# Kernel tuning notes

Measured on AMD Instinct MI355X. Metric: run time of the kernel, lower is better.

Reference implementation:

```python
import jax, jax.numpy as jnp
import numpy as np
from jax import lax

B, S, H = 2, 512, 2048          # batch, seq, hidden_size
I = 768                          # moe_intermediate_size
E = 64                           # num_experts
K = 8                            # num_experts_per_tok (top_k)


def setup_inputs() -> dict:
    key = jax.random.key(0)
    k1, k2, k3, k4 = jax.random.split(key, 4)
    hidden_states = jax.random.normal(k1, (B, S, H), jnp.float32)
    gate_weight = jax.random.normal(k2, (E, H), jnp.float32) * 0.02
    gate_up_weights = jax.random.normal(k3, (E, H, 2 * I), jnp.float32) * 0.02
    down_weights = jax.random.normal(k4, (E, I, H), jnp.float32) * 0.02
    return {
        "hidden_states": hidden_states,
        "gate_weight": gate_weight,
        "gate_up_weights": gate_up_weights,
        "down_weights": down_weights,
    }


def reference(hidden_states, gate_weight, gate_up_weights, down_weights):
    orig_shape = hidden_states.shape
    x = hidden_states.reshape(-1, H)          # [T, H]
    T = x.shape[0]

    # Router: softmax in fp32, top-k, renormalize (norm_topk_prob=True)
    logits = x @ gate_weight.T                # [T, E]
    probs = jax.nn.softmax(logits.astype(jnp.float32), axis=-1)
    routing_weights, selected_experts = lax.top_k(probs, K)   # [T, K]
    wsum = routing_weights.sum(axis=-1, keepdims=True)
    wsum = jnp.where(wsum == 0, 1.0, wsum)
    routing_weights = (routing_weights / wsum).astype(x.dtype)

    # Dense combine matrix [T, E]: zero weight for unselected experts.
    combine = jnp.zeros((T, E), x.dtype).at[
        jnp.arange(T)[:, None], selected_experts
    ].add(routing_weights)

    # Scan over experts; each step is one batched GEMM over all tokens,
    # masked/weighted by the combine weights (same math as per-token loop).
    def body(acc, ws):
        wgu, wd, we = ws                      # [H,2I], [I,H], [T]
        gu = x @ wgu                          # [T, 2I]
        gate, up = jnp.split(gu, 2, axis=-1)  # [T, I] each
        act = jax.nn.silu(gate) * up          # SwiGLU
        out = act @ wd                        # [T, H]
        return acc + we[:, None] * out, None

    init = jnp.zeros_like(x)
    final, _ = lax.scan(body, init, (gate_up_weights, down_weights, combine.T))
    return final.reshape(orig_shape)
```

## Files before the change

### kernel.cpp

```cpp
#include <hip/hip_runtime.h>
#include <hip/hip_bf16.h>
#include <hip/hip_fp16.h>

typedef unsigned int uint32;
typedef unsigned short u16;

#define TOK 1024
#define HID 2048
#define NEXP 64
#define TOPK 8
#define IMED 768
#define IMED2 1536

typedef __attribute__((ext_vector_type(8))) _Float16 half8;
typedef __attribute__((ext_vector_type(4))) float f32x4;

static __device__ __forceinline__ uint32 pack2(float a, float b) {
  union { _Float16 h[2]; uint32 u; } p;
  p.h[0] = (_Float16)a; p.h[1] = (_Float16)b;
  return p.u;
}
static __device__ __forceinline__ u16 f2h(float a) {
  union { _Float16 h; u16 u; } p;
  p.h = (_Float16)a;
  return p.u;
}

__global__ void xcast_kernel(const float* __restrict__ x, u16* __restrict__ xh) {
  size_t i = (size_t)blockIdx.x * 256 + threadIdx.x;
  const float4* p = (const float4*)(x + i * 8);
  float4 v0 = p[0], v1 = p[1];
  uint4 o;
  o.x = pack2(v0.x, v0.y); o.y = pack2(v0.z, v0.w);
  o.z = pack2(v1.x, v1.y); o.w = pack2(v1.z, v1.w);
  *(uint4*)(xh + i * 8) = o;
}

__global__ void router_kernel(const float* __restrict__ x, const float* __restrict__ gw,
                              int* __restrict__ topk_id, float* __restrict__ topk_w,
                              int* __restrict__ cnt) {
  int t = blockIdx.x;
  __shared__ __align__(16) float xs[HID];
  __shared__ float part[4][NEXP];
  const float* xr = x + (size_t)t * HID;
  for (int i = threadIdx.x; i < HID / 4; i += 256)
    ((float4*)xs)[i] = ((const float4*)xr)[i];
  __syncthreads();
  int e = threadIdx.x & 63, p = threadIdx.x >> 6;
  const float* wr = gw + (size_t)e * HID + p * 512;
  const float* xp = xs + p * 512;
  float s = 0.f;
  #pragma unroll 4
  for (int i = 0; i < 128; i++) {
    float4 w = ((const float4*)wr)[i];
    float4 xv = ((const float4*)xp)[i];
    s += w.x * xv.x + w.y * xv.y + w.z * xv.z + w.w * xv.w;
  }
  part[p][e] = s;
  __syncthreads();
  if (threadIdx.x < 64) {
    int l = threadIdx.x;
    float lg = part[0][l] + part[1][l] + part[2][l] + part[3][l];
    float m = lg;
    #pragma unroll
    for (int d = 1; d < 64; d <<= 1) m = fmaxf(m, __shfl_xor(m, d));
    float v = __expf(lg - m);
    float w8[TOPK]; int i8[TOPK]; float wsum = 0.f;
    #pragma unroll
    for (int k = 0; k < TOPK; k++) {
      float bv = v; int bi = l;
      #pragma unroll
      for (int d = 1; d < 64; d <<= 1) {
        float ov = __shfl_xor(bv, d);
        int oi = __shfl_xor(bi, d);
        if (ov > bv || (ov == bv && oi < bi)) { bv = ov; bi = oi; }
      }
      w8[k] = bv; i8[k] = bi; wsum += bv;
      if (l == bi) v = -1.f;
    }
    if (l == 0) {
      float rinv = 1.f / wsum;
      #pragma unroll
      for (int k = 0; k < TOPK; k++) {
        topk_id[t * TOPK + k] = i8[k];
        topk_w[t * TOPK + k] = w8[k] * rinv;
        atomicAdd(&cnt[i8[k]], 1);
      }
    }
  }
}

__global__ void scan_kernel(const int* __restrict__ cnt, int* __restrict__ off,
                            int* __restrict__ cur) {
  if (threadIdx.x == 0) {
    int a = 0;
    for (int e = 0; e < NEXP; e++) { off[e] = a; cur[e] = a; a += cnt[e]; }
    off[NEXP] = a;
  }
}

__global__ void scatter_kernel(const int* __restrict__ topk_id, const float* __restrict__ topk_w,
                               int* __restrict__ cur, int* __restrict__ row_tok,
                               float* __restrict__ row_w) {
  int i = blockIdx.x * 256 + threadIdx.x;
  int e = topk_id[i];
  int p = atomicAdd(&cur[e], 1);
  row_tok[p] = i >> 3;
  row_w[p] = topk_w[i];
}

__global__ __launch_bounds__(512, 2) void gateup_kernel(
    const u16* __restrict__ xh, const float* __restrict__ Wgu,
    const int* __restrict__ off, const int* __restrict__ row_tok,
    u16* __restrict__ act) {
  int bid = blockIdx.x;
  int xcd = bid & 7, s2 = bid >> 3;
  int e = xcd + ((s2 & 7) << 3);
  int slab = s2 >> 3;
  int r0 = off[e];
  int ne = off[e + 1] - r0;
  int c0 = slab * 96;

  __shared__ __align__(16) char AsB[256 * 80];
  __shared__ __align__(16) char BsB[192 * 80];

  int tid = threadIdx.x;
  int lane = tid & 63;
  int wid = tid >> 6;
  int wm = wid >> 1, wn = wid & 1;
  int fr = lane & 15, hi = lane >> 4;

  int arow = tid >> 1, aseg = tid & 1;
  int tok = row_tok[r0 + ((arow < ne) ? arow : 0)];
  const u16* xa = xh + (size_t)tok * HID + (aseg << 4);
  int axr = (arow >> 2) & 3;

  bool bact = tid < 384;
  int cg = tid % 24, h = (tid / 24) & 1, kq = tid / 48;
  int bcol = cg << 2;
  int gc = h ? (IMED + c0 + bcol) : (c0 + bcol);
  const float* wb = Wgu + (size_t)e * ((size_t)HID * IMED2) + (size_t)(kq << 2) * IMED2 + gc;
  int brbase = 96 * h + bcol;

  f32x4 accg[4][3], accu[4][3];
  #pragma unroll
  for (int a = 0; a < 4; a++)
    #pragma unroll
    for (int b = 0; b < 3; b++) { accg[a][b] = (f32x4)0.f; accu[a][b] = (f32x4)0.f; }

  uint4 qa0, qa1;
  float4 w0, w1, w2, w3;
  auto LOADT = [&]() {
    const uint4* p = (const uint4*)xa;
    qa0 = p[0]; qa1 = p[1];
    xa += 32;
    if (bact) {
      w0 = *(const float4*)(wb);
      w1 = *(const float4*)(wb + IMED2);
      w2 = *(const float4*)(wb + 2 * IMED2);
      w3 = *(const float4*)(wb + 3 * IMED2);
    }
    wb += (size_t)32 * IMED2;
  };
  auto STORET = [&]() {
    char* A_ = AsB + arow * 80;
    int g0 = aseg << 1;
    *(uint4*)(A_ + (((g0 + 0) ^ axr) << 4)) = qa0;
    *(uint4*)(A_ + (((g0 + 1) ^ axr) << 4)) = qa1;
    if (bact) {
      float c0v[4] = {w0.x, w0.y, w0.z, w0.w};
      float c1v[4] = {w1.x, w1.y, w1.z, w1.w};
      float c2v[4] = {w2.x, w2.y, w2.z, w2.w};
      float c3v[4] = {w3.x, w3.y, w3.z, w3.w};
      int kg = kq >> 1, kb = (kq & 1) << 3;
      #pragma unroll
      for (int cc = 0; cc < 4; cc++) {
        int br = brbase + cc;
        uint2 pv;
        pv.x = pack2(c0v[cc], c1v[cc]);
        pv.y = pack2(c2v[cc], c3v[cc]);
        *(uint2*)(BsB + br * 80 + (((kg ^ (br >> 2)) & 3) << 4) + kb) = pv;
      }
    }
  };

  const int NK = HID / 32;
  LOADT();
  STORET();
  LOADT();
  __syncthreads();

  for (int t = 0; t < NK; ++t) {
    half8 af[4];
    #pragma unroll
    for (int mi = 0; mi < 4; mi++) {
      int r = (wm << 6) + (mi << 4) + fr;
      af[mi] = *(half8*)(AsB + r * 80 + (((hi ^ (r >> 2)) & 3) << 4));
    }
    #pragma unroll
    for (int ni = 0; ni < 3; ni++) {
      int ng = (wn * 48) + (ni << 4) + fr;
      int nu = ng + 96;
      half8 bg = *(half8*)(BsB + ng * 80 + (((hi ^ (ng >> 2)) & 3) << 4));
      half8 bu = *(half8*)(BsB + nu * 80 + (((hi ^ (nu >> 2)) & 3) << 4));
      #pragma unroll
      for (int mi = 0; mi < 4; mi++) {
        accg[mi][ni] = __builtin_amdgcn_mfma_f32_16x16x32_f16(af[mi], bg, accg[mi][ni], 0, 0, 0);
        accu[mi][ni] = __builtin_amdgcn_mfma_f32_16x16x32_f16(af[mi], bu, accu[mi][ni], 0, 0, 0);
      }
    }
    __syncthreads();
    if (t + 1 < NK) {
      STORET();
      if (t + 2 < NK) LOADT();
      __syncthreads();
    }
  }

  #pragma unroll
  for (int mi = 0; mi < 4; mi++) {
    #pragma unroll
    for (int ni = 0; ni < 3; ni++) {
      int col = c0 + wn * 48 + (ni << 4) + fr;
      #pragma unroll
      for (int r = 0; r < 4; r++) {
        int rr = (wm << 6) + (mi << 4) + (hi << 2) + r;
        if (rr < ne) {
          float g = accg[mi][ni][r];
          float u = accu[mi][ni][r];
          float s = g / (1.f + __expf(-g)) * u;
          act[(size_t)(r0 + rr) * IMED + col] = f2h(s);
        }
      }
    }
  }
}

__global__ __launch_bounds__(512, 2) void down_kernel(
    const u16* __restrict__ act, const float* __restrict__ Wd,
    const int* __restrict__ off, const int* __restrict__ row_tok,
    const float* __restrict__ row_w, float* __restrict__ out) {
  int bid = blockIdx.x;
  int xcd = bid & 7, s2 = bid >> 3;
  int e = xcd + ((s2 & 7) << 3);
  int slab = s2 >> 3;
  int r0 = off[e];
  int ne = off[e + 1] - r0;
  int n0 = slab << 8;

  __shared__ __align__(16) char AsB[256 * 80];
  __shared__ __align__(16) char BsB[256 * 80];

  int tid = threadIdx.x;
  int lane = tid & 63;
  int wid = tid >> 6;
  int wm = wid >> 1, wn = wid & 1;
  int fr = lane & 15, hi = lane >> 4;

  int arow = tid >> 1, aseg = tid & 1;
  const u16* ap = act + (size_t)(r0 + ((arow < ne) ? arow : 0)) * IMED + (aseg << 4);
  int axr = (arow >> 2) & 3;

  int cq = tid & 63, kq = tid >> 6;
  int bcol = cq << 2;
  const float* wb = Wd + (size_t)e * ((size_t)IMED * HID) + (size_t)(kq << 2) * HID + n0 + bcol;

  f32x4 acc[4][8];
  #pragma unroll
  for (int a = 0; a < 4; a++)
    #pragma unroll
    for (int b = 0; b < 8; b++) acc[a][b] = (f32x4)0.f;

  uint4 qa0, qa1;
  float4 w0, w1, w2, w3;
  auto LOADT = [&]() {
    const uint4* p = (const uint4*)ap;
    qa0 = p[0]; qa1 = p[1];
    ap += 32;
    w0 = *(const float4*)(wb);
    w1 = *(const float4*)(wb + HID);
    w2 = *(const float4*)(wb + 2 * HID);
    w3 = *(const float4*)(wb + 3 * HID);
    wb += (size_t)32 * HID;
  };
  auto STORET = [&]() {
    char* A_ = AsB + arow * 80;
    int g0 = aseg << 1;
    *(uint4*)(A_ + (((g0 + 0) ^ axr) << 4)) = qa0;
    *(uint4*)(A_ + (((g0 + 1) ^ axr) << 4)) = qa1;
    float c0v[4] = {w0.x, w0.y, w0.z, w0.w};
    float c1v[4] = {w1.x, w1.y, w1.z, w1.w};
    float c2v[4] = {w2.x, w2.y, w2.z, w2.w};
    float c3v[4] = {w3.x, w3.y, w3.z, w3.w};
    int kg = kq >> 1, kb = (kq & 1) << 3;
    #pragma unroll
    for (int cc = 0; cc < 4; cc++) {
      int br = bcol + cc;
      uint2 pv;
      pv.x = pack2(c0v[cc], c1v[cc]);
      pv.y = pack2(c2v[cc], c3v[cc]);
      *(uint2*)(BsB + br * 80 + (((kg ^ (br >> 2)) & 3) << 4) + kb) = pv;
    }
  };

  const int NK = IMED / 32;
  LOADT();
  STORET();
  LOADT();
  __syncthreads();

  for (int t = 0; t < NK; ++t) {
    half8 af[4];
    #pragma unroll
    for (int mi = 0; mi < 4; mi++) {
      int r = (wm << 6) + (mi << 4) + fr;
      af[mi] = *(half8*)(AsB + r * 80 + (((hi ^ (r >> 2)) & 3) << 4));
    }
    #pragma unroll
    for (int ni = 0; ni < 8; ni++) {
      int n = (wn << 7) + (ni << 4) + fr;
      half8 bf_ = *(half8*)(BsB + n * 80 + (((hi ^ (n >> 2)) & 3) << 4));
      #pragma unroll
      for (int mi = 0; mi < 4; mi++)
        acc[mi][ni] = __builtin_amdgcn_mfma_f32_16x16x32_f16(af[mi], bf_, acc[mi][ni], 0, 0, 0);
    }
    __syncthreads();
    if (t + 1 < NK) {
      STORET();
      if (t + 2 < NK) LOADT();
      __syncthreads();
    }
  }

  #pragma unroll
  for (int mi = 0; mi < 4; mi++) {
    #pragma unroll
    for (int r = 0; r < 4; r++) {
      int rr = (wm << 6) + (mi << 4) + (hi << 2) + r;
      if (rr < ne) {
        float w = row_w[r0 + rr];
        int t = row_tok[r0 + rr];
        #pragma unroll
        for (int ni = 0; ni < 8; ni++) {
          int col = n0 + (wn << 7) + (ni << 4) + fr;
          unsafeAtomicAdd(&out[(size_t)t * HID + col], acc[mi][ni][r] * w);
        }
      }
    }
  }
}

extern "C" void kernel_launch(void* const* d_in, const int* in_sizes, int n_in,
                              void* d_out, int out_size, void* d_ws, size_t ws_size,
                              hipStream_t stream) {
  const float* x = (const float*)d_in[0];
  const float* gw = (const float*)d_in[1];
  const float* wgu = (const float*)d_in[2];
  const float* wd = (const float*)d_in[3];
  float* out = (float*)d_out;
  char* ws = (char*)d_ws;

  int* cnt = (int*)(ws + 0);
  int* cur = (int*)(ws + 256);
  int* off = (int*)(ws + 512);
  int* topk_id = (int*)(ws + 1024);
  float* topk_w = (float*)(ws + 1024 + 32768);
  int* row_tok = (int*)(ws + 1024 + 65536);
  float* row_w = (float*)(ws + 1024 + 98304);
  u16* act = (u16*)(ws + 135168);
  u16* xh = (u16*)(ws + 135168 + (size_t)TOK * TOPK * IMED * 2);

  hipMemsetAsync(cnt, 0, 256, stream);
  xcast_kernel<<<TOK * HID / 8 / 256, 256, 0, stream>>>(x, xh);
  router_kernel<<<TOK, 256, 0, stream>>>(x, gw, topk_id, topk_w, cnt);
  scan_kernel<<<1, 64, 0, stream>>>(cnt, off, cur);
  scatter_kernel<<<TOK * TOPK / 256, 256, 0, stream>>>(topk_id, topk_w, cur, row_tok, row_w);
  gateup_kernel<<<512, 512, 0, stream>>>(xh, wgu, off, row_tok, act);
  hipMemsetAsync(out, 0, (size_t)TOK * HID * sizeof(float), stream);
  down_kernel<<<512, 512, 0, stream>>>(act, wd, off, row_tok, row_w, out);
}
```

Before: 420.2 us.

## Fuse fp16 cast into router, batch 4 tokens per block, merge scan and scatter

The standalone x-to-fp16 cast kernel is folded into the router. Each router block now handles four tokens, so every gate-weight row it loads is reused across all four. The global-atomic count, scan and scatter steps are merged into one single-block kernel that counts and offsets in shared memory. This removes several launches and a memset from the pre-GEMM phase, but the single-block scatter serializes 8192 entries through one workgroup.

```diff
diff --git a/kernel.cpp b/kernel.cpp
--- a/kernel.cpp
+++ b/kernel.cpp
@@ -26,87 +26,93 @@
   return p.u;
 }
 
-__global__ void xcast_kernel(const float* __restrict__ x, u16* __restrict__ xh) {
-  size_t i = (size_t)blockIdx.x * 256 + threadIdx.x;
-  const float4* p = (const float4*)(x + i * 8);
-  float4 v0 = p[0], v1 = p[1];
-  uint4 o;
-  o.x = pack2(v0.x, v0.y); o.y = pack2(v0.z, v0.w);
-  o.z = pack2(v1.x, v1.y); o.w = pack2(v1.z, v1.w);
-  *(uint4*)(xh + i * 8) = o;
-}
-
-__global__ void router_kernel(const float* __restrict__ x, const float* __restrict__ gw,
-                              int* __restrict__ topk_id, float* __restrict__ topk_w,
-                              int* __restrict__ cnt) {
-  int t = blockIdx.x;
-  __shared__ __align__(16) float xs[HID];
-  __shared__ float part[4][NEXP];
-  const float* xr = x + (size_t)t * HID;
-  for (int i = threadIdx.x; i < HID / 4; i += 256)
-    ((float4*)xs)[i] = ((const float4*)xr)[i];
-  __syncthreads();
-  int e = threadIdx.x & 63, p = threadIdx.x >> 6;
-  const float* wr = gw + (size_t)e * HID + p * 512;
-  const float* xp = xs + p * 512;
-  float s = 0.f;
-  #pragma unroll 4
+__global__ __launch_bounds__(256) void router_kernel(
+    const float* __restrict__ x, const float* __restrict__ gw,
+    int* __restrict__ topk_id, float* __restrict__ topk_w,
+    u16* __restrict__ xh) {
+  int t0 = blockIdx.x << 2;
+  __shared__ float part[4][NEXP][5];
+  int tid = threadIdx.x;
+  int e = tid & 63, p = tid >> 6;
+  const float* gwp = gw + (size_t)e * HID + (p << 9);
+  const float* xp = x + (size_t)t0 * HID + (p << 9);
+  float acc[4] = {0.f, 0.f, 0.f, 0.f};
   for (int i = 0; i < 128; i++) {
-    float4 w = ((const float4*)wr)[i];
-    float4 xv = ((const float4*)xp)[i];
-    s += w.x * xv.x + w.y * xv.y + w.z * xv.z + w.w * xv.w;
-  }
-  part[p][e] = s;
-  __syncthreads();
-  if (threadIdx.x < 64) {
-    int l = threadIdx.x;
-    float lg = part[0][l] + part[1][l] + part[2][l] + part[3][l];
-    float m = lg;
-    #pragma unroll
-    for (int d = 1; d < 64; d <<= 1) m = fmaxf(m, __shfl_xor(m, d));
-    float v = __expf(lg - m);
-    float w8[TOPK]; int i8[TOPK]; float wsum = 0.f;
+    float4 w = ((const float4*)gwp)[i];
+    #pragma unroll
+    for (int t = 0; t < 4; t++) {
+      float4 xv = *(const float4*)(xp + (size_t)t * HID + (i << 2));
+      acc[t] += w.x * xv.x + w.y * xv.y + w.z * xv.z + w.w * xv.w;
+    }
+  }
+  #pragma unroll
+  for (int t = 0; t < 4; t++) part[p][e][t] = acc[t];
+  for (int i = tid; i < 2048; i += 256) {
+    int r = i >> 9;
+    int c = i & 511;
+    float4 v = *(const float4*)(x + (size_t)(t0 + r) * HID + (c << 2));
+    uint2 hp;
+    hp.x = pack2(v.x, v.y);
+    hp.y = pack2(v.z, v.w);
+    *(uint2*)(xh + (size_t)(t0 + r) * HID + (c << 2)) = hp;
+  }
+  __syncthreads();
+  int wv = tid >> 6, l = tid & 63;
+  int t = t0 + wv;
+  float lg = part[0][l][wv] + part[1][l][wv] + part[2][l][wv] + part[3][l][wv];
+  float m = lg;
+  #pragma unroll
+  for (int d = 1; d < 64; d <<= 1) m = fmaxf(m, __shfl_xor(m, d));
+  float v = __expf(lg - m);
+  float w8[TOPK]; int i8[TOPK]; float wsum = 0.f;
+  #pragma unroll
+  for (int k = 0; k < TOPK; k++) {
+    float bv = v; int bi = l;
+    #pragma unroll
+    for (int d = 1; d < 64; d <<= 1) {
+      float ov = __shfl_xor(bv, d);
+      int oi = __shfl_xor(bi, d);
+      if (ov > bv || (ov == bv && oi < bi)) { bv = ov; bi = oi; }
+    }
+    w8[k] = bv; i8[k] = bi; wsum += bv;
+    if (l == bi) v = -1.f;
+  }
+  if (l == 0) {
+    float rinv = 1.f / wsum;
     #pragma unroll
     for (int k = 0; k < TOPK; k++) {
-      float bv = v; int bi = l;
-      #pragma unroll
-      for (int d = 1; d < 64; d <<= 1) {
-        float ov = __shfl_xor(bv, d);
-        int oi = __shfl_xor(bi, d);
-        if (ov > bv || (ov == bv && oi < bi)) { bv = ov; bi = oi; }
-      }
-      w8[k] = bv; i8[k] = bi; wsum += bv;
-      if (l == bi) v = -1.f;
-    }
-    if (l == 0) {
-      float rinv = 1.f / wsum;
-      #pragma unroll
-      for (int k = 0; k < TOPK; k++) {
-        topk_id[t * TOPK + k] = i8[k];
-        topk_w[t * TOPK + k] = w8[k] * rinv;
-        atomicAdd(&cnt[i8[k]], 1);
-      }
-    }
-  }
-}
-
-__global__ void scan_kernel(const int* __restrict__ cnt, int* __restrict__ off,
-                            int* __restrict__ cur) {
-  if (threadIdx.x == 0) {
+      topk_id[t * TOPK + k] = i8[k];
+      topk_w[t * TOPK + k] = w8[k] * rinv;
+    }
+  }
+}
+
+__global__ __launch_bounds__(256) void scan_scatter_kernel(
+    const int* __restrict__ topk_id, const float* __restrict__ topk_w,
+    int* __restrict__ off, int* __restrict__ row_tok, float* __restrict__ row_w) {
+  __shared__ int scnt[NEXP];
+  __shared__ int soff[NEXP + 1];
+  __shared__ int scur[NEXP];
+  int tid = threadIdx.x;
+  if (tid < NEXP) scnt[tid] = 0;
+  __syncthreads();
+  for (int i = tid; i < TOK * TOPK; i += 256) atomicAdd(&scnt[topk_id[i]], 1);
+  __syncthreads();
+  if (tid == 0) {
     int a = 0;
-    for (int e = 0; e < NEXP; e++) { off[e] = a; cur[e] = a; a += cnt[e]; }
-    off[NEXP] = a;
-  }
-}
-
-__global__ void scatter_kernel(const int* __restrict__ topk_id, const float* __restrict__ topk_w,
-                               int* __restrict__ cur, int* __restrict__ row_tok,
-                               float* __restrict__ row_w) {
-  int i = blockIdx.x * 256 + threadIdx.x;
-  int e = topk_id[i];
-  int p = atomicAdd(&cur[e], 1);
-  row_tok[p] = i >> 3;
-  row_w[p] = topk_w[i];
+    for (int e = 0; e < NEXP; e++) { soff[e] = a; a += scnt[e]; }
+    soff[NEXP] = a;
+  }
+  __syncthreads();
+  if (tid < NEXP) scur[tid] = soff[tid];
+  __syncthreads();
+  for (int i = tid; i < TOK * TOPK; i += 256) {
+    int e = topk_id[i];
+    int p = atomicAdd(&scur[e], 1);
+    row_tok[p] = i >> 3;
+    row_w[p] = topk_w[i];
+  }
+  if (tid < NEXP + 1) off[tid] = soff[tid];
 }
 
 __global__ __launch_bounds__(512, 2) void gateup_kernel(
@@ -360,9 +366,7 @@
   float* out = (float*)d_out;
   char* ws = (char*)d_ws;
 
-  int* cnt = (int*)(ws + 0);
-  int* cur = (int*)(ws + 256);
-  int* off = (int*)(ws + 512);
+  int* off = (int*)(ws + 0);
   int* topk_id = (int*)(ws + 1024);
   float* topk_w = (float*)(ws + 1024 + 32768);
   int* row_tok = (int*)(ws + 1024 + 65536);
@@ -370,12 +374,9 @@
   u16* act = (u16*)(ws + 135168);
   u16* xh = (u16*)(ws + 135168 + (size_t)TOK * TOPK * IMED * 2);
 
-  hipMemsetAsync(cnt, 0, 256, stream);
-  xcast_kernel<<<TOK * HID / 8 / 256, 256, 0, stream>>>(x, xh);
-  router_kernel<<<TOK, 256, 0, stream>>>(x, gw, topk_id, topk_w, cnt);
-  scan_kernel<<<1, 64, 0, stream>>>(cnt, off, cur);
-  scatter_kernel<<<TOK * TOPK / 256, 256, 0, stream>>>(topk_id, topk_w, cur, row_tok, row_w);
+  router_kernel<<<TOK / 4, 256, 0, stream>>>(x, gw, topk_id, topk_w, xh);
+  scan_scatter_kernel<<<1, 256, 0, stream>>>(topk_id, topk_w, off, row_tok, row_w);
+  hipMemsetAsync(out, 0, (size_t)TOK * HID * sizeof(float), stream);
   gateup_kernel<<<512, 512, 0, stream>>>(xh, wgu, off, row_tok, act);
-  hipMemsetAsync(out, 0, (size_t)TOK * HID * sizeof(float), stream);
   down_kernel<<<512, 512, 0, stream>>>(act, wd, off, row_tok, row_w, out);
 }
```

Result: faster. 392.9 us (-6.5%).
